# Performance work log

Measured on AMD Instinct MI355X. Metric: run time of the kernel, lower is better.

Reference implementation:

```python
import jax, jax.numpy as jnp
import numpy as np


def _rope(x):
    # x: [B*, L, Dh] with Dh even
    L, Dh = x.shape[-2], x.shape[-1]
    inv = 1.0 / (10000.0 ** (jnp.arange(0, Dh, 2, dtype=jnp.float32) / Dh))
    freq = jnp.arange(L, dtype=jnp.float32)[:, None] * inv[None, :]  # [L, Dh/2]
    emb = jnp.concatenate([freq, freq], axis=-1)                     # [L, Dh]
    cos_, sin_ = jnp.cos(emb), jnp.sin(emb)
    half = Dh // 2
    x_rot = jnp.concatenate([-x[..., half:], x[..., :half]], axis=-1)
    return x * cos_ + x_rot * sin_


def setup_inputs() -> dict:
    key = jax.random.key(0)
    k1, k2, k3 = jax.random.split(key, 3)
    B, L, D = 2, 2048, 1024
    x = jax.random.normal(k1, (B, L, D), dtype=jnp.float32)
    key_mask = jnp.ones((B, L), dtype=jnp.int32)
    w_qkv = jax.random.normal(k2, (D, 3 * D), dtype=jnp.float32) * (D ** -0.5)
    w_proj = jax.random.normal(k3, (D, D), dtype=jnp.float32) * (D ** -0.5)
    return {"x": x, "key_mask": key_mask, "w_qkv": w_qkv, "w_proj": w_proj}


def reference(x, key_mask, w_qkv, w_proj):
    B, L, D = x.shape
    H = 16
    Dh = D // H
    scale = Dh ** -0.5
    qkv = (x @ w_qkv).reshape(B, L, 3, H, Dh).transpose(2, 0, 3, 1, 4)  # [3,B,H,L,Dh]
    q, k, v = qkv[0], qkv[1], qkv[2]
    q = _rope(q)
    k = _rope(k)
    sc = jnp.einsum('bhqd,bhkd->bhqk', q, k) * scale  # [B,H,L,L]
    sc = jnp.where(key_mask[:, None, None, :] == 0, -jnp.inf, sc)
    w = jax.nn.softmax(sc, axis=-1)
    out = jnp.einsum('bhqk,bhkd->bhqd', w, v)  # [B,H,L,Dh]
    out = out.transpose(0, 2, 1, 3).reshape(B, L, D)
    return out @ w_proj
```

## Files before the change

kernel.cpp:

```cpp
#include <hip/hip_runtime.h>
#include <hip/hip_bf16.h>
#include <math.h>


typedef __attribute__((ext_vector_type(8))) short bf16x8;
typedef __attribute__((ext_vector_type(4))) float f32x4;
typedef __attribute__((ext_vector_type(16))) float f32x16;

__device__ __forceinline__ unsigned short f2bf(float f) {
    union { float f; unsigned int u; } v; v.f = f;
    unsigned int u = v.u;
    return (unsigned short)((u + 0x7FFFu + ((u >> 16) & 1u)) >> 16);
}

__device__ __forceinline__ unsigned short bfc(float f) {
    union { __hip_bfloat16 h; unsigned short u; } c;
    c.h = __float2bfloat16(f);
    return c.u;
}

__device__ __forceinline__ unsigned cvtpk(float a, float b) {
    unsigned r;
    asm("v_cvt_pk_bf16_f32 %0, %1, %2" : "=v"(r) : "v"(a), "v"(b));
    return r;
}

__device__ __forceinline__ void gload_lds16(const unsigned short* g, unsigned short* l) {
    __builtin_amdgcn_global_load_lds(
        (const __attribute__((address_space(1))) void*)g,
        (__attribute__((address_space(3))) void*)l, 16, 0, 0);
}

__global__ __launch_bounds__(256) void prep_all(
    const float* __restrict__ x, const float* __restrict__ w_qkv, const float* __restrict__ w_proj,
    const int* __restrict__ mask,
    unsigned short* __restrict__ xsw, unsigned short* __restrict__ wqT,
    unsigned short* __restrict__ wpT, float2* __restrict__ tab,
    unsigned long long* __restrict__ mb)
{
    __shared__ unsigned short t[32][34];
    int bid = blockIdx.x, tid = threadIdx.x;
    if (bid < 2048) {
        int i = bid * 256 + tid;
        int row = i >> 7, blk = i & 127;
        int swblk = (blk & ~7) | ((blk ^ row) & 7);
        const float* src = x + ((size_t)row << 10) + (blk << 3);
        float4 f0 = *(const float4*)(src);
        float4 f1 = *(const float4*)(src + 4);
        ushort4 h0, h1;
        h0.x = f2bf(f0.x); h0.y = f2bf(f0.y); h0.z = f2bf(f0.z); h0.w = f2bf(f0.w);
        h1.x = f2bf(f1.x); h1.y = f2bf(f1.y); h1.z = f2bf(f1.z); h1.w = f2bf(f1.w);
        ushort4* dst = (ushort4*)(xsw + ((size_t)row << 10) + (swblk << 3));
        dst[0] = h0; dst[1] = h1;
    } else if (bid < 6144) {
        const float* w; unsigned short* wT; int Ncols, u;
        if (bid < 5120) { w = w_qkv; wT = wqT; Ncols = 3072; u = bid - 2048; }
        else            { w = w_proj; wT = wpT; Ncols = 1024; u = bid - 5120; }
        int NBx = Ncols >> 5;
        int n0 = (u % NBx) * 32, k0 = (u / NBx) * 32;
        int r = tid >> 3, c4 = (tid & 7) * 4;
        float4 f = *(const float4*)(w + (size_t)(k0 + r) * Ncols + n0 + c4);
        t[c4 + 0][r] = f2bf(f.x);
        t[c4 + 1][r] = f2bf(f.y);
        t[c4 + 2][r] = f2bf(f.z);
        t[c4 + 3][r] = f2bf(f.w);
        __syncthreads();
        ushort4 o;
        o.x = t[r][c4]; o.y = t[r][c4 + 1]; o.z = t[r][c4 + 2]; o.w = t[r][c4 + 3];
        int n = n0 + r, k = k0 + c4;
        int ksw = (k & ~63) | ((((k >> 3) ^ n) & 7) << 3) | (k & 7);
        *(ushort4*)(wT + (size_t)n * 1024 + ksw) = o;
    } else if (bid < 6400) {
        int i = (bid - 6144) * 256 + tid;
        int pos = i >> 5, d = i & 31;
        float inv = expf(-0.28782313662f * (float)d);
        float ang = (float)pos * inv;
        float s, c;
        sincosf(ang, &s, &c);
        tab[i] = make_float2(c, s);
    } else if (tid < 64) {
        int b = tid >> 5, w = tid & 31;
        unsigned long long bits = 0;
        #pragma unroll 8
        for (int j = 0; j < 64; ++j)
            if (mask[b * 2048 + w * 64 + j]) bits |= (1ULL << j);
        mb[tid] = bits;
    }
}

template<int MODE>
__global__ __launch_bounds__(256) void gemm_kernel(
    const unsigned short* __restrict__ Asw, const unsigned short* __restrict__ BT,
    const float2* __restrict__ ropetab,
    unsigned short* __restrict__ qb, unsigned short* __restrict__ kb,
    unsigned short* __restrict__ vb, float* __restrict__ Cout, int NB)
{
    const int K = 1024;
    __shared__ __align__(16) unsigned short As[128 * 64];
    __shared__ __align__(16) unsigned short Bs[64 * 64];
    int tid = threadIdx.x;
    int wid = tid >> 6, lane = tid & 63, lr = lane & 15, lg = lane >> 4;
    int wm = wid * 32;

    int per = NB * 4;
    int flat = blockIdx.x;
    int w = (flat & 7) * per + (flat >> 3);
    int row0 = (w / NB) * 128, col0 = (w % NB) * 64;

    int swk = (lr & 7) << 3;

    f32x4 acc[2][4];
    #pragma unroll
    for (int m = 0; m < 2; ++m)
        #pragma unroll
        for (int n = 0; n < 4; ++n)
            #pragma unroll
            for (int i = 0; i < 4; ++i) acc[m][n][i] = 0.0f;

    for (int k0 = 0; k0 < K; k0 += 64) {
        #pragma unroll
        for (int i = 0; i < 2; ++i) {
            int cbase = (i * 4 + wid) * 64;
            int c = cbase + lane;
            int r = c >> 3, cc = (c & 7) * 8;
            gload_lds16(BT + (size_t)(col0 + r) * K + k0 + cc, Bs + cbase * 8);
        }
        #pragma unroll
        for (int i = 0; i < 4; ++i) {
            int cbase = (i * 4 + wid) * 64;
            int c = cbase + lane;
            int r = c >> 3, cc = (c & 7) * 8;
            gload_lds16(Asw + (size_t)(row0 + r) * K + k0 + cc, As + cbase * 8);
        }
        __syncthreads();
        #pragma unroll
        for (int kk = 0; kk < 2; ++kk) {
            bf16x8 af[2], bfr[4];
            #pragma unroll
            for (int m = 0; m < 2; ++m)
                af[m] = *(const bf16x8*)(&As[(wm + m * 16 + lr) * 64 + ((kk * 32 + lg * 8) ^ swk)]);
            #pragma unroll
            for (int n = 0; n < 4; ++n)
                bfr[n] = *(const bf16x8*)(&Bs[(n * 16 + lr) * 64 + ((kk * 32 + lg * 8) ^ swk)]);
            #pragma unroll
            for (int m = 0; m < 2; ++m)
                #pragma unroll
                for (int n = 0; n < 4; ++n)
                    acc[m][n] = __builtin_amdgcn_mfma_f32_16x16x32_bf16(af[m], bfr[n], acc[m][n], 0, 0, 0);
        }
        __syncthreads();
    }

    if (MODE == 1) {
        int N = NB * 64;
        #pragma unroll
        for (int m = 0; m < 2; ++m)
            #pragma unroll
            for (int reg = 0; reg < 4; ++reg) {
                int grow = row0 + wm + m * 16 + lg * 4 + reg;
                #pragma unroll
                for (int n = 0; n < 4; ++n)
                    Cout[(size_t)grow * N + col0 + n * 16 + lr] = acc[m][n][reg];
            }
    } else {
        #pragma unroll
        for (int m = 0; m < 2; ++m)
            #pragma unroll
            for (int reg = 0; reg < 4; ++reg) {
                int grow = row0 + wm + m * 16 + lg * 4 + reg;
                int pos = grow & 2047;
                int bb = grow >> 11;
                #pragma unroll
                for (int n = 0; n < 4; ++n) {
                    int col = col0 + n * 16 + lr;
                    int part = col >> 10;
                    int h = (col >> 6) & 15;
                    int d = col & 63;
                    float v0 = acc[m][n][reg];
                    if (part == 2) {
                        int posl = (pos & 63) ^ ((d & 7) << 3);
                        vb[((size_t)bb * 16 + h) * 131072 + (size_t)d * 2048 + (pos & ~63) + posl] = f2bf(v0);
                    } else if (n < 2) {
                        float v1 = acc[m][n + 2][reg];
                        float2 cs = ropetab[pos * 32 + d];
                        size_t base = (((size_t)bb * 16 + h) * 2048 + pos) * 64;
                        float e0 = v0 * cs.x - v1 * cs.y;
                        float e1 = v1 * cs.x + v0 * cs.y;
                        if (part == 0) {
                            qb[base + d]      = f2bf(e0 * 0.18033688f);
                            qb[base + d + 32] = f2bf(e1 * 0.18033688f);
                        } else {
                            int sw = (pos & 7) << 3;
                            kb[base + (d ^ sw)]        = f2bf(e0);
                            kb[base + ((d + 32) ^ sw)] = f2bf(e1);
                        }
                    }
                }
            }
    }
}

__global__ __launch_bounds__(512, 2) void attn_kernel(
    const unsigned short* __restrict__ qbuf, const unsigned short* __restrict__ kbuf,
    const unsigned short* __restrict__ vtbuf, const unsigned long long* __restrict__ mbits,
    unsigned short* __restrict__ obuf)
{
    __shared__ __align__(16) unsigned short S[2][20480];

    int flat = blockIdx.x;
    int w = ((flat & 7) << 6) + (flat >> 3);
    int bh = w >> 4, qt = w & 15;
    int b = bh >> 4, h = bh & 15;
    int tid = threadIdx.x;
    int wid = tid >> 6;
    int half = wid >> 2, wq = wid & 3;
    int lane = tid & 63;
    int l31 = lane & 31, hi = lane >> 5, hi8 = hi << 3;
    int ht = tid & 255;
    int qrow0 = qt * 128 + wq * 32;
    const size_t bhbase = (size_t)bh * (2048 * 64);
    const unsigned short* kB = kbuf + bhbase + ((size_t)half << 16);
    const unsigned short* vt = vtbuf + bhbase;
    const unsigned long long* mw = mbits + (b << 5) + (half << 4);
    int swl = (l31 & 7) << 3;

    unsigned short* Kb = S[half];
    unsigned short* Vb = S[half] + 8192;

    bf16x8 qf[4];
    #pragma unroll
    for (int s = 0; s < 4; ++s)
        qf[s] = *(const bf16x8*)(qbuf + bhbase + (size_t)(qrow0 + l31) * 64 + s * 16 + hi8);

    f32x16 oacc[2];
    #pragma unroll
    for (int db = 0; db < 2; ++db)
        #pragma unroll
        for (int i = 0; i < 16; ++i) oacc[db][i] = 0.0f;
    float mrow = -INFINITY, lrow = 0.f;
    bf16x8 pfp[4];

    auto stage = [&](int t, int kbi, int vbi) {
        #pragma unroll
        for (int i = 0; i < 2; ++i) {
            int idx = i * 256 + ht;
            gload_lds16(kB + (size_t)t * 4096 + idx * 8, Kb + kbi * 4096 + i * 2048 + wq * 512);
            gload_lds16(vt + (size_t)(idx >> 3) * 2048 + (half * 16 + t) * 64 + (idx & 7) * 8,
                        Vb + vbi * 4096 + i * 2048 + wq * 512);
        }
    };

    int vc = 0, vn = 1, vp = 2;
    stage(0, 0, vc);
    #pragma unroll 1
    for (int t = 0; t < 16; ++t) {
        __syncthreads();
        if (t < 15) stage(t + 1, (t + 1) & 1, vn);
        unsigned long long bb = mw[t];
        const unsigned short* Kcur = Kb + (t & 1) * 4096;
        const unsigned short* Vprv = Vb + vp * 4096;

        __builtin_amdgcn_s_setprio(1);
        f32x16 sacc[2];
        #pragma unroll
        for (int ka = 0; ka < 2; ++ka)
            #pragma unroll
            for (int i = 0; i < 16; ++i) sacc[ka][i] = 0.0f;
        #pragma unroll
        for (int s = 0; s < 4; ++s)
            #pragma unroll
            for (int ka = 0; ka < 2; ++ka) {
                bf16x8 kfx = *(const bf16x8*)(Kcur + (ka * 32 + l31) * 64 + ((s * 16 + hi8) ^ swl));
                sacc[ka] = __builtin_amdgcn_mfma_f32_32x32x16_bf16(kfx, qf[s], sacc[ka], 0, 0, 0);
            }
        if (t) {
            #pragma unroll
            for (int s = 0; s < 4; ++s)
                #pragma unroll
                for (int db = 0; db < 2; ++db) {
                    bf16x8 vfx = *(const bf16x8*)(Vprv + (db * 32 + l31) * 64 + ((s * 16 + hi8) ^ swl));
                    oacc[db] = __builtin_amdgcn_mfma_f32_32x32x16_bf16(pfp[s], vfx, oacc[db], 0, 0, 0);
                }
        }
        __builtin_amdgcn_s_setprio(0);

        if (bb != ~0ULL) {
            int hi4 = hi << 2;
            #pragma unroll
            for (int kb2 = 0; kb2 < 2; ++kb2)
                #pragma unroll
                for (int reg = 0; reg < 16; ++reg) {
                    int kv = kb2 * 32 + (reg & 3) + ((reg >> 2) << 3) + hi4;
                    if (!((bb >> kv) & 1)) sacc[kb2][reg] = -1e30f;
                }
        }

        float tmax = sacc[0][0];
        #pragma unroll
        for (int kb2 = 0; kb2 < 2; ++kb2)
            #pragma unroll
            for (int reg = 0; reg < 16; ++reg)
                if (kb2 | reg) tmax = fmaxf(tmax, sacc[kb2][reg]);
        tmax = fmaxf(tmax, __shfl_xor(tmax, 32));

        if (__any(tmax > mrow + 8.f)) {
            float mnew = fmaxf(mrow, tmax);
            float sc = (mrow == -INFINITY) ? 0.f : __builtin_amdgcn_exp2f(mrow - mnew);
            lrow *= sc;
            mrow = mnew;
            #pragma unroll
            for (int reg = 0; reg < 16; ++reg) {
                int qof = (reg & 3) + ((reg >> 2) << 3) + (hi << 2);
                float scq = __shfl(sc, qof);
                oacc[0][reg] *= scq;
                oacc[1][reg] *= scq;
            }
        }

        float ps = 0.f;
        #pragma unroll
        for (int kb2 = 0; kb2 < 2; ++kb2)
            #pragma unroll
            for (int reg = 0; reg < 16; ++reg) {
                float pv = __builtin_amdgcn_exp2f(sacc[kb2][reg] - mrow);
                sacc[kb2][reg] = pv;
                ps += pv;
            }
        lrow += ps;

        #pragma unroll
        for (int s = 0; s < 4; ++s) {
            int kb2 = s >> 1, ra = (s & 1) * 8;
            unsigned wA0 = cvtpk(sacc[kb2][ra + 0], sacc[kb2][ra + 1]);
            unsigned wA1 = cvtpk(sacc[kb2][ra + 2], sacc[kb2][ra + 3]);
            unsigned wB0 = cvtpk(sacc[kb2][ra + 4], sacc[kb2][ra + 5]);
            unsigned wB1 = cvtpk(sacc[kb2][ra + 6], sacc[kb2][ra + 7]);
            asm("v_permlane32_swap_b32 %0, %1" : "+v"(wA0), "+v"(wB0));
            asm("v_permlane32_swap_b32 %0, %1" : "+v"(wA1), "+v"(wB1));
            union { unsigned u[4]; bf16x8 v; } pk;
            pk.u[0] = wA0; pk.u[1] = wA1; pk.u[2] = wB0; pk.u[3] = wB1;
            pfp[s] = pk.v;
        }

        int tmp = vp; vp = vc; vc = vn; vn = tmp;
    }

    {
        const unsigned short* Vprv = Vb + vp * 4096;
        #pragma unroll
        for (int s = 0; s < 4; ++s)
            #pragma unroll
            for (int db = 0; db < 2; ++db) {
                bf16x8 vfx = *(const bf16x8*)(Vprv + (db * 32 + l31) * 64 + ((s * 16 + hi8) ^ swl));
                oacc[db] = __builtin_amdgcn_mfma_f32_32x32x16_bf16(pfp[s], vfx, oacc[db], 0, 0, 0);
            }
    }
    lrow += __shfl_xor(lrow, 32);

    __syncthreads();
    float* xO = (float*)&S[0][0];
    float* xm = xO + 8448;
    float* xl = xm + 256;
    if (half == 1) {
        float* dst = xO + (wq * 64 + lane) * 33;
        #pragma unroll
        for (int db = 0; db < 2; ++db)
            #pragma unroll
            for (int reg = 0; reg < 16; ++reg)
                dst[db * 16 + reg] = oacc[db][reg];
        xm[wq * 64 + lane] = mrow;
        xl[wq * 64 + lane] = lrow;
    }
    __syncthreads();
    if (half == 0) {
        float m1 = xm[wq * 64 + lane];
        float l1 = xl[wq * 64 + lane];
        float mst = fmaxf(mrow, m1);
        float a0 = (mrow == -INFINITY) ? 0.f : __builtin_amdgcn_exp2f(mrow - mst);
        float a1 = (m1 == -INFINITY) ? 0.f : __builtin_amdgcn_exp2f(m1 - mst);
        float lst = lrow * a0 + l1 * a1;
        const float* src = xO + (wq * 64 + lane) * 33;
        #pragma unroll
        for (int reg = 0; reg < 16; ++reg) {
            int qof = (reg & 3) + ((reg >> 2) << 3) + (hi << 2);
            float s0 = __shfl(a0, qof);
            float s1 = __shfl(a1, qof);
            float li = 1.0f / __shfl(lst, qof);
            int qrow = qrow0 + qof;
            int qsw = qrow & 7;
            #pragma unroll
            for (int db = 0; db < 2; ++db) {
                float val = (oacc[db][reg] * s0 + src[db * 16 + reg] * s1) * li;
                int dcol = db * 32 + l31;
                int jj = dcol >> 3;
                int colsw = h * 64 + (((jj ^ qsw) & 7) << 3) + (dcol & 7);
                obuf[((size_t)b * 2048 + qrow) * 1024 + colsw] = bfc(val);
            }
        }
    }
}

extern "C" void kernel_launch(void* const* d_in, const int* in_sizes, int n_in,
                              void* d_out, int out_size, void* d_ws, size_t ws_size,
                              hipStream_t stream) {
    const float* x      = (const float*)d_in[0];
    const int* key_mask = (const int*)d_in[1];
    const float* w_qkv  = (const float*)d_in[2];
    const float* w_proj = (const float*)d_in[3];
    float* out = (float*)d_out;

    char* ws = (char*)d_ws;
    unsigned short* qb  = (unsigned short*)(ws);
    unsigned short* kb  = (unsigned short*)(ws + 8388608);
    unsigned short* vtb = (unsigned short*)(ws + 16777216);
    unsigned short* xob = (unsigned short*)(ws + 25165824);
    unsigned short* wqT = (unsigned short*)(ws + 33554432);
    unsigned short* wpT = (unsigned short*)(ws + 39845888);
    float2*         tab = (float2*)(ws + 41943040);
    unsigned long long* mb = (unsigned long long*)(ws + 42467328);

    dim3 blk(256);
    prep_all<<<dim3(6401), blk, 0, stream>>>(x, w_qkv, w_proj, key_mask, xob, wqT, wpT, tab, mb);
    gemm_kernel<0><<<dim3(1536), blk, 0, stream>>>(xob, wqT, tab, qb, kb, vtb, nullptr, 48);
    attn_kernel<<<dim3(512), dim3(512), 0, stream>>>(qb, kb, vtb, mb, xob);
    gemm_kernel<1><<<dim3(512), blk, 0, stream>>>(xob, wpT, nullptr, nullptr, nullptr, nullptr, out, 16);
}
```

Before: 128.1 us.

## Drop deferred PV software pipelining and use double-buffered V in-iteration

Removes the one-iteration-delayed P·V MFMA scheme, which needed a triple-buffered V in LDS and carried P fragments across iterations. P·V now runs in the same iteration right after softmax, with V double-buffered alongside K, so LDS per block shrinks. This frees LDS and registers, but it loses the overlap of the P·V MFMAs with the QK and softmax work of the next tile.

```diff
diff --git a/kernel.cpp b/kernel.cpp
--- a/kernel.cpp
+++ b/kernel.cpp
@@ -205,7 +205,7 @@
     const unsigned short* __restrict__ vtbuf, const unsigned long long* __restrict__ mbits,
     unsigned short* __restrict__ obuf)
 {
-    __shared__ __align__(16) unsigned short S[2][20480];
+    __shared__ __align__(16) unsigned short S[2][16384];
 
     int flat = blockIdx.x;
     int w = ((flat & 7) << 6) + (flat >> 3);
@@ -238,27 +238,26 @@
         #pragma unroll
         for (int i = 0; i < 16; ++i) oacc[db][i] = 0.0f;
     float mrow = -INFINITY, lrow = 0.f;
-    bf16x8 pfp[4];
-
-    auto stage = [&](int t, int kbi, int vbi) {
+
+    auto stage = [&](int t) {
+        int bi = t & 1;
         #pragma unroll
         for (int i = 0; i < 2; ++i) {
             int idx = i * 256 + ht;
-            gload_lds16(kB + (size_t)t * 4096 + idx * 8, Kb + kbi * 4096 + i * 2048 + wq * 512);
+            gload_lds16(kB + (size_t)t * 4096 + idx * 8, Kb + bi * 4096 + i * 2048 + wq * 512);
             gload_lds16(vt + (size_t)(idx >> 3) * 2048 + (half * 16 + t) * 64 + (idx & 7) * 8,
-                        Vb + vbi * 4096 + i * 2048 + wq * 512);
+                        Vb + bi * 4096 + i * 2048 + wq * 512);
         }
     };
 
-    int vc = 0, vn = 1, vp = 2;
-    stage(0, 0, vc);
+    stage(0);
     #pragma unroll 1
     for (int t = 0; t < 16; ++t) {
         __syncthreads();
-        if (t < 15) stage(t + 1, (t + 1) & 1, vn);
+        if (t < 15) stage(t + 1);
         unsigned long long bb = mw[t];
         const unsigned short* Kcur = Kb + (t & 1) * 4096;
-        const unsigned short* Vprv = Vb + vp * 4096;
+        const unsigned short* Vcur = Vb + (t & 1) * 4096;
 
         __builtin_amdgcn_s_setprio(1);
         f32x16 sacc[2];
@@ -273,15 +272,6 @@
                 bf16x8 kfx = *(const bf16x8*)(Kcur + (ka * 32 + l31) * 64 + ((s * 16 + hi8) ^ swl));
                 sacc[ka] = __builtin_amdgcn_mfma_f32_32x32x16_bf16(kfx, qf[s], sacc[ka], 0, 0, 0);
             }
-        if (t) {
-            #pragma unroll
-            for (int s = 0; s < 4; ++s)
-                #pragma unroll
-                for (int db = 0; db < 2; ++db) {
-                    bf16x8 vfx = *(const bf16x8*)(Vprv + (db * 32 + l31) * 64 + ((s * 16 + hi8) ^ swl));
-                    oacc[db] = __builtin_amdgcn_mfma_f32_32x32x16_bf16(pfp[s], vfx, oacc[db], 0, 0, 0);
-                }
-        }
         __builtin_amdgcn_s_setprio(0);
 
         if (bb != ~0ULL) {
@@ -328,6 +318,7 @@
             }
         lrow += ps;
 
+        bf16x8 pf[4];
         #pragma unroll
         for (int s = 0; s < 4; ++s) {
             int kb2 = s >> 1, ra = (s & 1) * 8;
@@ -339,22 +330,19 @@
             asm("v_permlane32_swap_b32 %0, %1" : "+v"(wA1), "+v"(wB1));
             union { unsigned u[4]; bf16x8 v; } pk;
             pk.u[0] = wA0; pk.u[1] = wA1; pk.u[2] = wB0; pk.u[3] = wB1;
-            pfp[s] = pk.v;
-        }
-
-        int tmp = vp; vp = vc; vc = vn; vn = tmp;
-    }
-
-    {
-        const unsigned short* Vprv = Vb + vp * 4096;
+            pf[s] = pk.v;
+        }
+        __builtin_amdgcn_s_setprio(1);
         #pragma unroll
         for (int s = 0; s < 4; ++s)
             #pragma unroll
             for (int db = 0; db < 2; ++db) {
-                bf16x8 vfx = *(const bf16x8*)(Vprv + (db * 32 + l31) * 64 + ((s * 16 + hi8) ^ swl));
-                oacc[db] = __builtin_amdgcn_mfma_f32_32x32x16_bf16(pfp[s], vfx, oacc[db], 0, 0, 0);
-            }
-    }
+                bf16x8 vfx = *(const bf16x8*)(Vcur + (db * 32 + l31) * 64 + ((s * 16 + hi8) ^ swl));
+                oacc[db] = __builtin_amdgcn_mfma_f32_32x32x16_bf16(pf[s], vfx, oacc[db], 0, 0, 0);
+            }
+        __builtin_amdgcn_s_setprio(0);
+    }
+
     lrow += __shfl_xor(lrow, 32);
 
     __syncthreads();
```

Result: no change. 129.5 us (+1.1%).
